# Kernel tuning notes

Hardware: AMD Instinct MI355X
Metric: run time of the kernel (lower is better)

Reference implementation:

```python
import jax, jax.numpy as jnp
import numpy as np

FS = 48000
RIR_LENGTH = 96000
FILTER_LENGTH = 1023          # odd, so hilbert_one_sided works: N = 2*F - 1
N_FREQ = (FILTER_LENGTH + 1) // 2   # 512 rfft bins
SHARPNESS = 8.0
EPS = 1e-9
# strictly increasing fit-frequency bin indices (10 bands, like surface_freqs/dir_freqs)
FREQ_IDX = np.array([1, 2, 4, 8, 16, 32, 64, 128, 256, 480])


def get_interpolator(n_freq_target, fi):
    """numpy port of the torch get_interpolator (precomputed constant)."""
    fi = np.asarray(fi)
    r = np.zeros((len(fi), n_freq_target), np.float32)
    d = np.diff(fi)
    for i in range(len(fi)):
        if i == 0:
            r[0, :fi[1]] = np.concatenate([np.ones(fi[0]), 1 - np.arange(d[0]) / d[0]])
        elif i == len(fi) - 1:
            r[i, fi[i - 1]:] = np.concatenate([np.arange(d[i - 1]) / d[i - 1], np.ones(n_freq_target - fi[i])])
        else:
            r[i, fi[i - 1]:fi[i + 1]] = np.concatenate([np.arange(d[i - 1]) / d[i - 1], 1 - np.arange(d[i]) / d[i]])
    return r


def fibonacci_sphere(n):
    i = np.arange(n, dtype=np.float64)
    phi = np.pi * (np.sqrt(5.0) - 1.0)
    y = 1 - i / (n - 1) * 2
    rad = np.sqrt(np.maximum(1 - y * y, 0.0))
    th = phi * i
    return np.stack([np.cos(th) * rad, y, np.sin(th) * rad], -1).astype(np.float32)


def safe_log(x):
    return jnp.log(jnp.where(x <= EPS, EPS, x))


def hilbert_one_sided(x):
    """Minimum phase from log-magnitude. x: [..., F] with N = 2F-1 odd."""
    F = x.shape[-1]
    N = 2 * F - 1
    Xf = jnp.fft.irfft(x, n=N, axis=-1)
    h = jnp.concatenate([jnp.ones((1,), x.dtype),
                         2.0 * jnp.ones(((N + 1) // 2 - 1,), x.dtype),
                         jnp.zeros((N - (N + 1) // 2,), x.dtype)])
    return jnp.imag(jnp.fft.rfft(Xf * h, axis=-1))


def setup_inputs() -> dict:
    key = jax.random.key(0)
    ks = jax.random.split(key, 6)
    B, P, S, NF = 8, 4096, 16, 128
    interp = get_interpolator(N_FREQ, FREQ_IDX)  # [10, 512]
    return {
        "surface_params": jax.random.normal(ks[0], (S, len(FREQ_IDX)), jnp.float32),
        "dir_params": jax.random.normal(ks[1], (NF, len(FREQ_IDX)), jnp.float32),
        "path_dirs": jax.random.normal(ks[2], (B, P, 3), jnp.float32),
        "source_kernel": jax.random.normal(ks[3], (FILTER_LENGTH,), jnp.float32) * 0.02,
        "surf_interp": jnp.asarray(interp),
        "dir_interp": jnp.asarray(interp),
        "fib_points": jnp.asarray(fibonacci_sphere(NF)),
        "mask": jax.random.randint(ks[4], (B, P, S), 0, 3, jnp.int32),
        "delays": jax.random.randint(ks[5], (B, P), 100, RIR_LENGTH - FILTER_LENGTH - 1, jnp.int32),
    }


def reference(surface_params, dir_params, path_dirs, source_kernel,
              surf_interp, dir_interp, fib_points, mask, delays):
    B, P, _ = path_dirs.shape
    # --- per-path surface reflection log-magnitude at fit frequencies ---
    log_refl = safe_log(jax.nn.sigmoid(surface_params))            # [S, Fs]
    log_amp_s = jnp.einsum('bps,sf->bpf', mask.astype(jnp.float32), log_refl)  # [B,P,Fs]
    # --- source directivity via fibonacci-sphere softmax weighting ---
    d = path_dirs / (jnp.linalg.norm(path_dirs, axis=-1, keepdims=True) + EPS)
    w = jax.nn.softmax(SHARPNESS * jnp.einsum('bpc,nc->bpn', d, fib_points), axis=-1)  # [B,P,N]
    log_amp_d = safe_log(jnp.einsum('bpn,nf->bpf', w, jax.nn.sigmoid(dir_params)))     # [B,P,Fd]
    # --- interpolate to full frequency grid (precomputed linterp matmuls) ---
    log_amp = (jnp.einsum('bpf,fq->bpq', log_amp_s, surf_interp) +
               jnp.einsum('bpf,fq->bpq', log_amp_d, dir_interp))   # [B,P,512]
    # --- minimum phase + irfft -> per-reflection filters ---
    phase = hilbert_one_sided(log_amp)
    fr = jnp.exp(log_amp) * jnp.exp(-1j * phase)                    # complex64 [B,P,512]
    filt = jnp.fft.irfft(fr, n=FILTER_LENGTH, axis=-1)              # [B,P,1023]
    # --- 1/distance attenuation and scatter into RIR at times of arrival ---
    gains = 1.0 / jnp.maximum(delays.astype(jnp.float32) / 48.0, 1.0)  # [B,P]
    idx = delays[..., None] + jnp.arange(FILTER_LENGTH)[None, None, :]  # [B,P,L]
    rows = jnp.arange(B)[:, None, None]
    rir = jnp.zeros((B, RIR_LENGTH), jnp.float32).at[rows, idx].add(filt * gains[..., None])
    # --- convolve with learned source response kernel ('same') ---
    pad = (FILTER_LENGTH - 1) // 2
    out = jax.lax.conv_general_dilated(rir[:, None, :], source_kernel[None, None, :],
                                       window_strides=(1,), padding=[(pad, pad)],
                                       dimension_numbers=('NCH', 'OIH', 'NCH'))
    return out[:, 0, :]  # [B, RIR_LENGTH]
```

## Files before the change

kernel.cpp:

```cpp
#include <hip/hip_runtime.h>
#include <math.h>

#define N_FFTC    1023
#define NFREQ     512
#define NBANDS    10
#define NPATH     32768
#define NSURF     16
#define NDIR      128
#define RIR_LEN   96000
#define FILT_LEN  1023
#define TWO_PI_D  6.283185307179586476925286766559
#define BS        1024
#define NBINS     93

typedef _Float16 f16x8 __attribute__((ext_vector_type(8)));
typedef float    f32x4 __attribute__((ext_vector_type(4)));

#define AS1 __attribute__((address_space(1)))
#define AS3 __attribute__((address_space(3)))
__device__ __forceinline__ void gload16(const void* g, void* l) {
    __builtin_amdgcn_global_load_lds((const AS1 void*)g, (AS3 void*)l, 16, 0, 0);
}

#define WS_WT     0UL
#define WS_TWC    2097152UL
#define WS_TWS    2105344UL
#define WS_LOGR   2113536UL
#define WS_SIGD   2114560UL
#define WS_GS     2119680UL
#define WS_GD     2160640UL
#define WS_TBL    2201600UL
#define WS_WB     2283520UL
#define WS_A      8378368UL

__global__ void k0a_tables(const float* __restrict__ sp, const float* __restrict__ dp,
                           double* __restrict__ twc, double* __restrict__ tws,
                           float* __restrict__ logr, float* __restrict__ sigd)
{
    int idx = blockIdx.x * 256 + threadIdx.x;
    if (idx < 1023) {
        double ang = TWO_PI_D * (double)idx / 1023.0;
        twc[idx] = cos(ang);
        tws[idx] = sin(ang);
    } else if (idx >= 1024 && idx < 1024 + NSURF * NBANDS) {
        int i = idx - 1024;
        float s = 1.f / (1.f + expf(-sp[i]));
        logr[i] = logf(s <= 1e-9f ? 1e-9f : s);
    } else if (idx >= 2048 && idx < 2048 + NDIR * NBANDS) {
        int i = idx - 2048;
        sigd[i] = 1.f / (1.f + expf(-dp[i]));
    }
}

__global__ void k0b_G(const float* __restrict__ SI, const float* __restrict__ DI,
                      const double* __restrict__ twc,
                      double* __restrict__ Gs, double* __restrict__ Gd)
{
    int idx = blockIdx.x * 256 + threadIdx.x;
    if (idx >= NBANDS * NFREQ) return;
    int f = idx >> 9, n = idx & 511;
    double gs = 0.0, gd = 0.0;
    for (int m = 0; m < NFREQ; ++m) {
        double c = (m == 0) ? 1.0 : 2.0;
        double t = c * twc[(m * n) % 1023];
        gs += t * (double)SI[f * NFREQ + m];
        gd += t * (double)DI[f * NFREQ + m];
    }
    Gs[idx] = gs;
    Gd[idx] = gd;
}

__global__ void k0c_TBL(const double* __restrict__ tws,
                        const double* __restrict__ Gs, const double* __restrict__ Gd,
                        const float* __restrict__ SI, const float* __restrict__ DI,
                        float4* __restrict__ TBL)
{
    int idx = blockIdx.x * 256 + threadIdx.x;
    if (idx >= NBANDS * NFREQ) return;
    int f = idx >> 9, k = idx & 511;
    double ps = 0.0, pd_ = 0.0;
    for (int n = 1; n < 512; ++n) {
        double s = tws[(k * n) % 1023];
        ps  += s * Gs[f * NFREQ + n];
        pd_ += s * Gd[f * NFREQ + n];
    }
    double sc = -2.0 / 1023.0;
    float4 v;
    v.x = SI[idx];
    v.y = DI[idx];
    v.z = (float)(sc * ps);
    v.w = (float)(sc * pd_);
    TBL[idx] = v;
}

__global__ void k0d_W(const double* __restrict__ twc, const double* __restrict__ tws,
                      _Float16* __restrict__ WThi)
{
    int idx = blockIdx.x * 256 + threadIdx.x;
    int t = idx >> 10, k = idx & 1023;
    double v = 0.0;
    if (t < 1023) {
        if (k < 512) v = (((k == 0) ? 1.0 : 2.0) / 1023.0) * twc[(k * t) % 1023];
        else         v = (2.0 / 1023.0) * tws[((k - 512) * t) % 1023];
    }
    WThi[idx] = (_Float16)((float)(v * 16384.0));
}

__device__ __forceinline__ float wave_sum64(float v) {
#pragma unroll
    for (int m = 1; m < 64; m <<= 1) v += __shfl_xor(v, m, 64);
    return v;
}
__device__ __forceinline__ float wave_max64(float v) {
#pragma unroll
    for (int m = 1; m < 64; m <<= 1) v = fmaxf(v, __shfl_xor(v, m, 64));
    return v;
}

__global__ __launch_bounds__(256) void k1_ab(
    const float* __restrict__ path_dirs, const float* __restrict__ fib,
    const int* __restrict__ mask, const int* __restrict__ delays,
    const float* __restrict__ logr, const float* __restrict__ sigd,
    const float4* __restrict__ TBL,
    _Float16* __restrict__ A, int chunkStart, int m)
{
    __shared__ float pbs[4][4][22];
    int wave = threadIdx.x >> 6, lane = threadIdx.x & 63;
    int pb = blockIdx.x * 16 + wave * 4;

    int n0 = lane, n1 = lane + 64;
    float fx0 = fib[n0 * 3], fy0 = fib[n0 * 3 + 1], fz0 = fib[n0 * 3 + 2];
    float fx1 = fib[n1 * 3], fy1 = fib[n1 * 3 + 1], fz1 = fib[n1 * 3 + 2];

    for (int pp = 0; pp < 4; ++pp) {
        int pg = chunkStart + pb + pp;
        float dx = path_dirs[pg * 3 + 0], dy = path_dirs[pg * 3 + 1], dz = path_dirs[pg * 3 + 2];
        float inv = 1.f / (sqrtf(dx * dx + dy * dy + dz * dz) + 1e-9f);
        dx *= inv; dy *= inv; dz *= inv;
        float l0 = 8.f * (dx * fx0 + dy * fy0 + dz * fz0);
        float l1 = 8.f * (dx * fx1 + dy * fy1 + dz * fz1);
        float mx = wave_max64(fmaxf(l0, l1));
        float e0 = __expf(l0 - mx), e1 = __expf(l1 - mx);
        float ssum = wave_sum64(e0 + e1);
        float w0 = e0 / ssum, w1 = e1 / ssum;

        float lad[10];
#pragma unroll
        for (int f = 0; f < NBANDS; ++f) {
            float part = wave_sum64(w0 * sigd[n0 * NBANDS + f] + w1 * sigd[n1 * NBANDS + f]);
            lad[f] = __logf(part <= 1e-9f ? 1e-9f : part);
        }

        float las[10];
#pragma unroll
        for (int f = 0; f < NBANDS; ++f) las[f] = 0.f;
        const int* mrow = mask + (size_t)pg * NSURF;
#pragma unroll
        for (int s = 0; s < NSURF; ++s) {
            float mv = (float)mrow[s];
#pragma unroll
            for (int f = 0; f < NBANDS; ++f) las[f] += mv * logr[s * NBANDS + f];
        }

        int dly = delays[pg];
        float g = 1.f / fmaxf((float)dly / 48.f, 1.f);

        if (lane == 0) {
#pragma unroll
            for (int f = 0; f < NBANDS; ++f) {
                pbs[wave][pp][f]      = las[f];
                pbs[wave][pp][10 + f] = lad[f];
            }
            pbs[wave][pp][20] = g * 16384.f;
        }
    }

    for (int i = 0; i < 8; ++i) {
        int q = i * 64 + lane;
        float4 t[10];
#pragma unroll
        for (int f = 0; f < NBANDS; ++f) t[f] = TBL[f * NFREQ + q];
#pragma unroll
        for (int pp = 0; pp < 4; ++pp) {
            float la = 0.f, ph = 0.f;
#pragma unroll
            for (int f = 0; f < NBANDS; ++f) {
                float ls  = pbs[wave][pp][f];
                float ld_ = pbs[wave][pp][10 + f];
                la += ls * t[f].x + ld_ * t[f].y;
                ph += ls * t[f].z + ld_ * t[f].w;
            }
            float M = pbs[wave][pp][20] * __expf(la);
            float sn, cs;
            __sincosf(ph, &sn, &cs);
            _Float16* row = A + (size_t)(pb + pp) * 1024;
            row[q]       = (_Float16)(M * cs);
            row[512 + q] = (_Float16)(M * sn);
        }
    }
}

#define NKT 16
__global__ __launch_bounds__(512) void k2_gemm(
    const _Float16* __restrict__ A, const _Float16* __restrict__ WT,
    float* __restrict__ filt)
{
    extern __shared__ __align__(16) char smem[];

    int nwg = gridDim.x, bid = blockIdx.x;
    int swzb = (nwg & 7) ? bid : ((bid & 7) * (nwg >> 3) + (bid >> 3));
    int rowTile = swzb >> 2, colTile = swzb & 3;
    int p0 = rowTile * 256, t0 = colTile * 256;

    int tid = threadIdx.x, lane = tid & 63, wid = tid >> 6;
    int wr = wid >> 2, wc = wid & 3;
    int li = lane & 15, lg = lane >> 4, xr = li & 7;

    int srow = tid >> 3;
    int slot = (tid & 7) ^ (srow & 7);
    char* dstbase = smem + (tid & ~63) * 16;

    f32x4 acc[8][4];
#pragma unroll
    for (int i = 0; i < 8; ++i)
#pragma unroll
        for (int j = 0; j < 4; ++j) acc[i][j] = (f32x4){0.f, 0.f, 0.f, 0.f};

    auto stage = [&](int c, int hs, int kt) {
        int kk = (kt & 15) << 6;
        int off = kk + slot * 8;
        char* dst = dstbase + c * 65536 + ((hs >= 2) ? 32768 : 0) + (hs & 1) * 16384;
        if (hs < 2) {
            const _Float16* g0 = A + (size_t)(p0 + (hs & 1) * 128 + srow) * 1024 + off;
            gload16(g0, dst);
            gload16(g0 + (size_t)64 * 1024, dst + 8192);
        } else {
            const _Float16* g0 = WT + (size_t)(t0 + (hs & 1) * 128 + srow) * 1024 + off;
            gload16(g0, dst);
            gload16(g0 + (size_t)64 * 1024, dst + 8192);
        }
    };

#pragma unroll
    for (int hs = 0; hs < 4; ++hs) stage(0, hs, 0);

    int browLocal0 = (wc & 1) * 64;

    for (int kt = 0; kt < NKT; ++kt) {
        int c = kt & 1;
        int ktn = (kt + 1 < NKT) ? (kt + 1) : 0;
        const char* bufA = smem + c * 65536 + wr * 16384;
        const char* bufB = smem + c * 65536 + 32768 + (wc >> 1) * 16384;

        f16x8 bf[4][2];
#pragma unroll
        for (int ph = 0; ph < 4; ++ph) {
            stage(c ^ 1, ph, ktn);
            if (ph == 0) asm volatile("s_waitcnt vmcnt(2)" ::: "memory");
            __builtin_amdgcn_s_barrier();

            f16x8 af[2][2];
#pragma unroll
            for (int m2 = 0; m2 < 2; ++m2) {
                int row = (ph * 2 + m2) * 16 + li;
#pragma unroll
                for (int ks = 0; ks < 2; ++ks)
                    af[m2][ks] = *(const f16x8*)(bufA + row * 128 + (((ks * 4 + lg) ^ xr) << 4));
            }
            if (ph == 0) {
#pragma unroll
                for (int n = 0; n < 4; ++n) {
                    int row = browLocal0 + n * 16 + li;
#pragma unroll
                    for (int ks = 0; ks < 2; ++ks)
                        bf[n][ks] = *(const f16x8*)(bufB + row * 128 + (((ks * 4 + lg) ^ xr) << 4));
                }
            }
            __builtin_amdgcn_s_setprio(1);
#pragma unroll
            for (int m2 = 0; m2 < 2; ++m2)
#pragma unroll
                for (int n = 0; n < 4; ++n)
#pragma unroll
                    for (int ks = 0; ks < 2; ++ks)
                        acc[ph * 2 + m2][n] = __builtin_amdgcn_mfma_f32_16x16x32_f16(
                            af[m2][ks], bf[n][ks], acc[ph * 2 + m2][n], 0, 0, 0);
            __builtin_amdgcn_s_setprio(0);
            __builtin_amdgcn_s_barrier();
        }
    }

    const float dsc = 1.f / (16384.f * 16384.f);
#pragma unroll
    for (int m = 0; m < 8; ++m) {
        int prow = p0 + wr * 128 + m * 16 + lg * 4;
#pragma unroll
        for (int r = 0; r < 4; ++r) {
            float* fp = filt + (size_t)(prow + r) * 1024 + t0 + wc * 64 + li;
#pragma unroll
            for (int n = 0; n < 4; ++n)
                fp[n * 16] = acc[m][n][r] * dsc;
        }
    }
}

#define SKW(j) ((j) + ((j) >> 5))
__global__ __launch_bounds__(256) void k4_scatter(
    const float* __restrict__ filt, const int* __restrict__ delays,
    float* __restrict__ WB, int chunkStart, int m)
{
    __shared__ float win4[4][2112];
    int b = blockIdx.y, bin = blockIdx.x;
    int binStart = bin << 10;
    int wid = threadIdx.x >> 6, lane = threadIdx.x & 63;

    for (int i = lane; i < 2112; i += 64) win4[wid][i] = 0.f;

    float* w = win4[wid];
    auto ACC = [&](int off, float4 v0, float4 v1, float4 v2, float4 v3) {
        int j = off + lane * 4;
        w[SKW(j + 0)] += v0.x; w[SKW(j + 1)] += v0.y; w[SKW(j + 2)] += v0.z; w[SKW(j + 3)] += v0.w;
        j += 256;
        w[SKW(j + 0)] += v1.x; w[SKW(j + 1)] += v1.y; w[SKW(j + 2)] += v1.z; w[SKW(j + 3)] += v1.w;
        j += 256;
        w[SKW(j + 0)] += v2.x; w[SKW(j + 1)] += v2.y; w[SKW(j + 2)] += v2.z; w[SKW(j + 3)] += v2.w;
        j += 256;
        w[SKW(j + 0)] += v3.x; w[SKW(j + 1)] += v3.y; w[SKW(j + 2)] += v3.z; w[SKW(j + 3)] += v3.w;
    };

    int lo = b * 4096, hi = lo + 4096;
    if (lo < chunkStart) lo = chunkStart;
    if (hi > chunkStart + m) hi = chunkStart + m;

    for (int base = lo + wid * 64; base < hi; base += 256) {
        int p = base + lane;
        int d = (p < hi) ? delays[p] : -1;
        bool match = (d >= binStart) && (d < binStart + BS);
        unsigned long long mask = __ballot(match);
        while (mask) {
            int bit0 = __ffsll(mask) - 1; mask &= mask - 1;
            bool has2 = (mask != 0);
            int bit1 = bit0;
            if (has2) { bit1 = __ffsll(mask) - 1; mask &= mask - 1; }
            int off0 = __shfl(d, bit0) - binStart;
            int off1 = __shfl(d, bit1) - binStart;
            const float4* fr0 = (const float4*)(filt + (size_t)(base + bit0 - chunkStart) * 1024);
            const float4* fr1 = (const float4*)(filt + (size_t)(base + bit1 - chunkStart) * 1024);
            float4 a0 = fr0[lane], a1 = fr0[64 + lane], a2 = fr0[128 + lane], a3 = fr0[192 + lane];
            if (has2) {
                float4 b0 = fr1[lane], b1 = fr1[64 + lane], b2 = fr1[128 + lane], b3 = fr1[192 + lane];
                ACC(off0, a0, a1, a2, a3);
                ACC(off1, b0, b1, b2, b3);
            } else {
                ACC(off0, a0, a1, a2, a3);
            }
        }
    }
    __syncthreads();

    float* wb = WB + ((size_t)b * NBINS + bin) * 2048;
    if (chunkStart == 0) {
        for (int i = threadIdx.x; i < 2048; i += 256)
            wb[i] = win4[0][SKW(i)] + win4[1][SKW(i)] + win4[2][SKW(i)] + win4[3][SKW(i)];
    } else {
        for (int i = threadIdx.x; i < 2048; i += 256)
            wb[i] += win4[0][SKW(i)] + win4[1][SKW(i)] + win4[2][SKW(i)] + win4[3][SKW(i)];
    }
}

#define SEG 2048
#define SK(i) ((i) + ((i) >> 5))
__global__ __launch_bounds__(256) void k3_conv(
    const float* __restrict__ WB, const float* __restrict__ kern, float* __restrict__ out)
{
    __shared__ float rs[3184];
    __shared__ float ks[FILT_LEN];
    int b = blockIdx.y;
    int t0 = blockIdx.x * SEG;
    const float* wbb = WB + (size_t)b * NBINS * 2048;
    for (int i = threadIdx.x; i < FILT_LEN; i += 256) ks[i] = kern[i];
    for (int i = threadIdx.x; i < SEG + FILT_LEN - 1 + 8; i += 256) {
        int t = t0 - 511 + i;
        float v = 0.f;
        if (t >= 0 && t < RIR_LEN) {
            int bn = t >> 10, o = t & 1023;
            if (bn < NBINS) v = wbb[bn * 2048 + o];
            if (bn >= 1)    v += wbb[(bn - 1) * 2048 + o + 1024];
        }
        rs[SK(i)] = v;
    }
    __syncthreads();

    int base = threadIdx.x * 8;
    float a0 = 0.f, a1 = 0.f, a2 = 0.f, a3 = 0.f, a4 = 0.f, a5 = 0.f, a6 = 0.f, a7 = 0.f;
    float w0 = rs[SK(base + 0)], w1 = rs[SK(base + 1)], w2 = rs[SK(base + 2)], w3 = rs[SK(base + 3)];
    float w4 = rs[SK(base + 4)], w5 = rs[SK(base + 5)], w6 = rs[SK(base + 6)], w7 = rs[SK(base + 7)];
#pragma unroll 8
    for (int k = 0; k < FILT_LEN; ++k) {
        float kv = ks[k];
        a0 = fmaf(kv, w0, a0); a1 = fmaf(kv, w1, a1);
        a2 = fmaf(kv, w2, a2); a3 = fmaf(kv, w3, a3);
        a4 = fmaf(kv, w4, a4); a5 = fmaf(kv, w5, a5);
        a6 = fmaf(kv, w6, a6); a7 = fmaf(kv, w7, a7);
        w0 = w1; w1 = w2; w2 = w3; w3 = w4; w4 = w5; w5 = w6; w6 = w7;
        w7 = rs[SK(base + k + 8)];
    }
    int t = t0 + base;
    size_t ob = (size_t)b * RIR_LEN;
    if (t + 7 < RIR_LEN) {
        float4 v0 = {a0, a1, a2, a3}, v1 = {a4, a5, a6, a7};
        *(float4*)&out[ob + t]     = v0;
        *(float4*)&out[ob + t + 4] = v1;
    } else {
        float av[8] = {a0, a1, a2, a3, a4, a5, a6, a7};
        for (int j = 0; j < 8; ++j)
            if (t + j < RIR_LEN) out[ob + t + j] = av[j];
    }
}

extern "C" void kernel_launch(void* const* d_in, const int* in_sizes, int n_in,
                              void* d_out, int out_size, void* d_ws, size_t ws_size,
                              hipStream_t stream)
{
    const float* surface_params = (const float*)d_in[0];
    const float* dir_params     = (const float*)d_in[1];
    const float* path_dirs      = (const float*)d_in[2];
    const float* source_kernel  = (const float*)d_in[3];
    const float* surf_interp    = (const float*)d_in[4];
    const float* dir_interp     = (const float*)d_in[5];
    const float* fib_points     = (const float*)d_in[6];
    const int*   mask           = (const int*)d_in[7];
    const int*   delays         = (const int*)d_in[8];
    float* out = (float*)d_out;
    char*  ws  = (char*)d_ws;

    _Float16*  WT   = (_Float16*)(ws + WS_WT);
    double*    twc  = (double*)(ws + WS_TWC);
    double*    tws  = (double*)(ws + WS_TWS);
    float*     logr = (float*)(ws + WS_LOGR);
    float*     sigd = (float*)(ws + WS_SIGD);
    double*    Gs   = (double*)(ws + WS_GS);
    double*    Gd   = (double*)(ws + WS_GD);
    float4*    TBL  = (float4*)(ws + WS_TBL);
    float*     WB   = (float*)(ws + WS_WB);
    _Float16*  A    = (_Float16*)(ws + WS_A);

    (void)hipFuncSetAttribute((const void*)k2_gemm,
                              hipFuncAttributeMaxDynamicSharedMemorySize, 131072);

    size_t abCap = (ws_size > WS_A) ? (ws_size - WS_A) : 0;
    long long cm = (long long)((abCap / 6144) & ~(size_t)255);
    if (cm > NPATH) cm = NPATH;
    if (cm < 256)   cm = 256;
    int chunkM = (int)cm;
    float* filt = (float*)(ws + WS_A + (size_t)chunkM * 2048);

    k0a_tables<<<16, 256, 0, stream>>>(surface_params, dir_params, twc, tws, logr, sigd);
    k0b_G     <<<20, 256, 0, stream>>>(surf_interp, dir_interp, twc, Gs, Gd);
    k0c_TBL   <<<20, 256, 0, stream>>>(tws, Gs, Gd, surf_interp, dir_interp, TBL);
    k0d_W     <<<4096, 256, 0, stream>>>(twc, tws, WT);

    for (int cs = 0; cs < NPATH; cs += chunkM) {
        int m = NPATH - cs;
        if (m > chunkM) m = chunkM;
        k1_ab<<<m / 16, 256, 0, stream>>>(path_dirs, fib_points, mask, delays,
                                          logr, sigd, TBL, A, cs, m);
        k2_gemm<<<(m / 256) * 4, 512, 131072, stream>>>(A, WT, filt);
        dim3 g4(NBINS, 8);
        k4_scatter<<<g4, 256, 0, stream>>>(filt, delays, WB, cs, m);
    }

    dim3 g3((RIR_LEN + SEG - 1) / SEG, 8);
    k3_conv<<<g3, 256, 0, stream>>>(WB, source_kernel, out);
}
```

Baseline: 365.0 us.

## Split per-path band computation from spectrum generation into separate kernels

The fused k1 kernel is split in two. k1a computes the per-path log-amplitude band coefficients and gain once for all paths into a global buffer. k1b then generates the fp16 spectrum rows with one thread per frequency bin, keeping the TBL entries in registers across 64 paths. This is meant to raise parallelism and reuse of the table loads in the spectrum stage, at the cost of an extra kernel launch and a global round trip for the per-path parameters.

```diff
diff --git a/kernel.cpp b/kernel.cpp
--- a/kernel.cpp
+++ b/kernel.cpp
@@ -31,7 +31,8 @@
 #define WS_GD     2160640UL
 #define WS_TBL    2201600UL
 #define WS_WB     2283520UL
-#define WS_A      8378368UL
+#define WS_PB     8378368UL
+#define WS_A      11524096UL
 
 __global__ void k0a_tables(const float* __restrict__ sp, const float* __restrict__ dp,
                            double* __restrict__ twc, double* __restrict__ tws,
@@ -117,23 +118,21 @@
     return v;
 }
 
-__global__ __launch_bounds__(256) void k1_ab(
+__global__ __launch_bounds__(256) void k1a_band(
     const float* __restrict__ path_dirs, const float* __restrict__ fib,
     const int* __restrict__ mask, const int* __restrict__ delays,
     const float* __restrict__ logr, const float* __restrict__ sigd,
-    const float4* __restrict__ TBL,
-    _Float16* __restrict__ A, int chunkStart, int m)
-{
-    __shared__ float pbs[4][4][22];
+    float* __restrict__ PB)
+{
     int wave = threadIdx.x >> 6, lane = threadIdx.x & 63;
-    int pb = blockIdx.x * 16 + wave * 4;
+    int pbase = blockIdx.x * 16 + wave * 4;
 
     int n0 = lane, n1 = lane + 64;
     float fx0 = fib[n0 * 3], fy0 = fib[n0 * 3 + 1], fz0 = fib[n0 * 3 + 2];
     float fx1 = fib[n1 * 3], fy1 = fib[n1 * 3 + 1], fz1 = fib[n1 * 3 + 2];
 
     for (int pp = 0; pp < 4; ++pp) {
-        int pg = chunkStart + pb + pp;
+        int pg = pbase + pp;
         float dx = path_dirs[pg * 3 + 0], dy = path_dirs[pg * 3 + 1], dz = path_dirs[pg * 3 + 2];
         float inv = 1.f / (sqrtf(dx * dx + dy * dy + dz * dz) + 1e-9f);
         dx *= inv; dy *= inv; dz *= inv;
@@ -166,37 +165,44 @@
         float g = 1.f / fmaxf((float)dly / 48.f, 1.f);
 
         if (lane == 0) {
+            float* pr = PB + (size_t)pg * 24;
 #pragma unroll
             for (int f = 0; f < NBANDS; ++f) {
-                pbs[wave][pp][f]      = las[f];
-                pbs[wave][pp][10 + f] = lad[f];
+                pr[f]      = las[f];
+                pr[10 + f] = lad[f];
             }
-            pbs[wave][pp][20] = g * 16384.f;
-        }
-    }
-
-    for (int i = 0; i < 8; ++i) {
-        int q = i * 64 + lane;
-        float4 t[10];
-#pragma unroll
-        for (int f = 0; f < NBANDS; ++f) t[f] = TBL[f * NFREQ + q];
-#pragma unroll
-        for (int pp = 0; pp < 4; ++pp) {
-            float la = 0.f, ph = 0.f;
-#pragma unroll
-            for (int f = 0; f < NBANDS; ++f) {
-                float ls  = pbs[wave][pp][f];
-                float ld_ = pbs[wave][pp][10 + f];
-                la += ls * t[f].x + ld_ * t[f].y;
-                ph += ls * t[f].z + ld_ * t[f].w;
-            }
-            float M = pbs[wave][pp][20] * __expf(la);
-            float sn, cs;
-            __sincosf(ph, &sn, &cs);
-            _Float16* row = A + (size_t)(pb + pp) * 1024;
-            row[q]       = (_Float16)(M * cs);
-            row[512 + q] = (_Float16)(M * sn);
-        }
+            pr[20] = g * 16384.f;
+        }
+    }
+}
+
+__global__ __launch_bounds__(512) void k1b_ab(
+    const float4* __restrict__ TBL, const float* __restrict__ PB,
+    _Float16* __restrict__ A, int chunkStart)
+{
+    int q = threadIdx.x;
+    int pb0 = blockIdx.x * 64;
+
+    float4 t[10];
+#pragma unroll
+    for (int f = 0; f < NBANDS; ++f) t[f] = TBL[f * NFREQ + q];
+
+    for (int j = 0; j < 64; ++j) {
+        const float* pr = PB + (size_t)(chunkStart + pb0 + j) * 24;
+        float la = 0.f, ph = 0.f;
+#pragma unroll
+        for (int f = 0; f < NBANDS; ++f) {
+            float ls  = pr[f];
+            float ld_ = pr[10 + f];
+            la += ls * t[f].x + ld_ * t[f].y;
+            ph += ls * t[f].z + ld_ * t[f].w;
+        }
+        float M = pr[20] * __expf(la);
+        float sn, cs;
+        __sincosf(ph, &sn, &cs);
+        _Float16* row = A + (size_t)(pb0 + j) * 1024;
+        row[q]       = (_Float16)(M * cs);
+        row[512 + q] = (_Float16)(M * sn);
     }
 }
 
@@ -443,6 +449,7 @@
     double*    Gd   = (double*)(ws + WS_GD);
     float4*    TBL  = (float4*)(ws + WS_TBL);
     float*     WB   = (float*)(ws + WS_WB);
+    float*     PB   = (float*)(ws + WS_PB);
     _Float16*  A    = (_Float16*)(ws + WS_A);
 
     (void)hipFuncSetAttribute((const void*)k2_gemm,
@@ -459,12 +466,13 @@
     k0b_G     <<<20, 256, 0, stream>>>(surf_interp, dir_interp, twc, Gs, Gd);
     k0c_TBL   <<<20, 256, 0, stream>>>(tws, Gs, Gd, surf_interp, dir_interp, TBL);
     k0d_W     <<<4096, 256, 0, stream>>>(twc, tws, WT);
+    k1a_band  <<<NPATH / 16, 256, 0, stream>>>(path_dirs, fib_points, mask, delays,
+                                               logr, sigd, PB);
 
     for (int cs = 0; cs < NPATH; cs += chunkM) {
         int m = NPATH - cs;
         if (m > chunkM) m = chunkM;
-        k1_ab<<<m / 16, 256, 0, stream>>>(path_dirs, fib_points, mask, delays,
-                                          logr, sigd, TBL, A, cs, m);
+        k1b_ab<<<m / 64, 512, 0, stream>>>(TBL, PB, A, cs);
         k2_gemm<<<(m / 256) * 4, 512, 131072, stream>>>(A, WT, filt);
         dim3 g4(NBINS, 8);
         k4_scatter<<<g4, 256, 0, stream>>>(filt, delays, WB, cs, m);
```

After: 365.3 us (median of 2 runs). No clear change (+0.1%).
